# Performance work log

Measured on AMD Instinct MI355X. Metric: run time of the kernel, lower is better.

## Reference

```python
import jax, jax.numpy as jnp
import numpy as np

B, S, D = 1, 2048, 2048
NH, NKV, HD = 32, 8, 64
EPS = 1e-5
SCALE = float(HD) ** 0.5


def _rope(x, cos, sin):
    # x: [b, h, s, hd]; cos/sin: [s, hd//2]; interleaved-pair rotary (executorch style)
    xr = x[..., 0::2]
    xi = x[..., 1::2]
    c = cos[None, None, :, :]
    s = sin[None, None, :, :]
    out_r = xr * c - xi * s
    out_i = xr * s + xi * c
    return jnp.stack([out_r, out_i], axis=-1).reshape(x.shape)


def _rmsnorm(x, w):
    var = jnp.mean(x * x, axis=-1, keepdims=True)
    return x * jax.lax.rsqrt(var + EPS) * w


def setup_inputs() -> dict:
    key = jax.random.key(0)
    ks = jax.random.split(key, 6)
    hidden_states = jax.random.normal(ks[0], (B, S, D), dtype=jnp.float32)
    # standard Llama rope tables, theta=10000
    inv_freq = 1.0 / (10000.0 ** (np.arange(0, HD, 2, dtype=np.float32) / HD))
    t = np.arange(S, dtype=np.float32)
    ang = np.outer(t, inv_freq)  # [S, HD//2]
    freqs_cos = jnp.asarray(np.cos(ang), dtype=jnp.float32)
    freqs_sin = jnp.asarray(np.sin(ang), dtype=jnp.float32)
    # additive causal mask [1,1,S,S]
    causal = jnp.tril(jnp.ones((S, S), dtype=bool))
    atten_mask = jnp.where(causal, 0.0, -1e9).astype(jnp.float32)[None, None]
    sd = 1.0 / np.sqrt(D)
    wq = jax.random.normal(ks[1], (NH * HD, D), dtype=jnp.float32) * sd
    wk = jax.random.normal(ks[2], (NKV * HD, D), dtype=jnp.float32) * sd
    wv = jax.random.normal(ks[3], (NKV * HD, D), dtype=jnp.float32) * sd
    wo = jax.random.normal(ks[4], (D, NH * HD), dtype=jnp.float32) * sd
    q_norm_w = jnp.ones((HD,), dtype=jnp.float32)
    k_norm_w = jnp.ones((HD,), dtype=jnp.float32)
    return dict(hidden_states=hidden_states, freqs_cos=freqs_cos, freqs_sin=freqs_sin,
                atten_mask=atten_mask, wq=wq, wk=wk, wv=wv, wo=wo,
                q_norm_w=q_norm_w, k_norm_w=k_norm_w)


def reference(hidden_states, freqs_cos, freqs_sin, atten_mask, wq, wk, wv, wo, q_norm_w, k_norm_w):
    b, s, _ = hidden_states.shape
    n_rep = NH // NKV
    # fused QKV projections (Linear: x @ W.T)
    q = (hidden_states @ wq.T).reshape(b, s, NH, HD).transpose(0, 2, 1, 3)   # [b,nh,s,hd]
    k = (hidden_states @ wk.T).reshape(b, s, NKV, HD).transpose(0, 2, 1, 3)  # [b,nkv,s,hd]
    v = (hidden_states @ wv.T).reshape(b, s, NKV, HD).transpose(0, 2, 1, 3)
    # RoPE, then QK RMSNorm (qk_norm_before_rope=False)
    q = _rope(q, freqs_cos, freqs_sin)
    k = _rope(k, freqs_cos, freqs_sin)
    q = _rmsnorm(q, q_norm_w)
    k = _rmsnorm(k, k_norm_w)
    # no KV cache (prefill): kh = k^T, vh = v, then GQA repeat
    kh = jnp.repeat(k, n_rep, axis=1)  # [b,nh,s,hd]
    vh = jnp.repeat(v, n_rep, axis=1)
    attn = jnp.einsum('bhqd,bhkd->bhqk', q, kh) / SCALE
    attn = jax.nn.softmax(attn + atten_mask, axis=-1)
    y = jnp.einsum('bhqk,bhkd->bhqd', attn, vh)
    y = y.transpose(0, 2, 1, 3).reshape(b, s, NH * HD)
    y = y @ wo.T
    # module returns (y, [kh], [vh]); kh stored transposed (b,nh,hd,s)
    return (y, kh.transpose(0, 1, 3, 2), vh)
```

## Files before the change

kernel.cpp:

```cpp
#include <hip/hip_runtime.h>
#include <cstdint>
#include <cstddef>

#define S_   2048
#define D_   2048
#define NH_  32
#define NKV_ 8
#define HD_  64

using bf16x8 = __attribute__((ext_vector_type(8))) __bf16;
using f32x4  = __attribute__((ext_vector_type(4))) float;

#define AS_GLOBAL(p) (const __attribute__((address_space(1))) void*)(p)
#define AS_LDS(p)    (__attribute__((address_space(3))) void*)(p)

__device__ __forceinline__ float b2f(uint u) {
  union { uint u; float f; } c; c.u = u << 16; return c.f;
}

__global__ __launch_bounds__(256) void cvt_all(
    const float* __restrict__ hs, const float* __restrict__ wq,
    const float* __restrict__ wk, const float* __restrict__ wv,
    const float* __restrict__ wo,
    __bf16* __restrict__ hs_bf, __bf16* __restrict__ wq_bf,
    __bf16* __restrict__ wk_bf, __bf16* __restrict__ wv_bf,
    __bf16* __restrict__ wo_bf) {
#pragma unroll
  for (int p = 0; p < 4; ++p) {
    int i = blockIdx.x * 1024 + p * 256 + threadIdx.x;
    const float* src; __bf16* dst; int base;
    if (i < 1048576)      { src = hs; dst = hs_bf; base = 0; }
    else if (i < 2097152) { src = wq; dst = wq_bf; base = 1048576; }
    else if (i < 2359296) { src = wk; dst = wk_bf; base = 2097152; }
    else if (i < 2621440) { src = wv; dst = wv_bf; base = 2359296; }
    else                  { src = wo; dst = wo_bf; base = 2621440; }
    i -= base;
    const float4 v = reinterpret_cast<const float4*>(src)[i];
    __bf16 t[4] = {(__bf16)v.x, (__bf16)v.y, (__bf16)v.z, (__bf16)v.w};
    reinterpret_cast<uint2*>(dst)[i] = *reinterpret_cast<uint2*>(t);
  }
}

__device__ __forceinline__ void gemm_compute_step(
    const char* ldsA, const char* ldsB, f32x4 (&acc)[4][4],
    int l15, int lg, int wm, int wn) {
  bf16x8 af[4][2], bfr[4][2];
#pragma unroll
  for (int f = 0; f < 4; ++f) {
    const int arow = wm*64 + f*16 + l15;
    const int brow = wn*64 + f*16 + l15;
#pragma unroll
    for (int ks = 0; ks < 2; ++ks) {
      af[f][ks] = *reinterpret_cast<const bf16x8*>(
          ldsA + arow*128 + (((ks*4 + lg) ^ (arow & 7)) << 4));
      bfr[f][ks] = *reinterpret_cast<const bf16x8*>(
          ldsB + brow*128 + (((ks*4 + lg) ^ (brow & 7)) << 4));
    }
  }
#pragma unroll
  for (int mf = 0; mf < 4; ++mf)
#pragma unroll
    for (int nf = 0; nf < 4; ++nf) {
      acc[mf][nf] = __builtin_amdgcn_mfma_f32_16x16x32_bf16(
          af[mf][0], bfr[nf][0], acc[mf][nf], 0, 0, 0);
      acc[mf][nf] = __builtin_amdgcn_mfma_f32_16x16x32_bf16(
          af[mf][1], bfr[nf][1], acc[mf][nf], 0, 0, 0);
    }
}

template <int MODE>
__device__ __forceinline__ void gemm_tile_128_bf(
    char (*lds)[32768],
    const __bf16* __restrict__ A, const __bf16* __restrict__ B,
    __bf16* __restrict__ C, int K, int N, int m0, int n0,
    const float* __restrict__ cosT, const float* __restrict__ sinT,
    const float* __restrict__ nw) {
  const int tid = threadIdx.x;
  const int l = tid & 63;
  const int w = tid >> 6;
  const int l15 = l & 15, lg = l >> 4;
  const int wm = w >> 1, wn = w & 1;

  f32x4 acc[4][4] = {};

  const int srow   = tid >> 3;
  const int schunk = (tid & 7) ^ (srow & 7);
  const __bf16* gA = A + (size_t)(m0 + srow) * K + schunk * 8;
  const __bf16* gB = B + (size_t)(n0 + srow) * K + schunk * 8;
  const int ldst = tid * 16;
  const int nt = K >> 6;

  auto stage = [&](char* buf, int k0) {
#pragma unroll
    for (int i = 0; i < 4; ++i) {
      __builtin_amdgcn_global_load_lds(AS_GLOBAL(gA + (size_t)i*32*K + k0),
                                       AS_LDS(buf + i*4096 + ldst), 16, 0, 0);
      __builtin_amdgcn_global_load_lds(AS_GLOBAL(gB + (size_t)i*32*K + k0),
                                       AS_LDS(buf + 16384 + i*4096 + ldst), 16, 0, 0);
    }
  };

  stage(&lds[0][0], 0);
  stage(&lds[1][0], 64);

  for (int t = 0; t < nt; ++t) {
    if (t + 1 < nt) asm volatile("s_waitcnt vmcnt(8)" ::: "memory");
    else            asm volatile("s_waitcnt vmcnt(0)" ::: "memory");
    __builtin_amdgcn_s_barrier();

    gemm_compute_step(&lds[t & 1][0], &lds[t & 1][16384], acc, l15, lg, wm, wn);

    __builtin_amdgcn_s_barrier();

    if (t + 2 < nt) stage(&lds[t & 1][0], (t + 2) * 64);
  }

  if constexpr (MODE == 0) {
#pragma unroll
    for (int mf = 0; mf < 4; ++mf)
#pragma unroll
      for (int nf = 0; nf < 4; ++nf)
#pragma unroll
        for (int r = 0; r < 4; ++r)
          C[(size_t)(m0 + wm*64 + mf*16 + lg*4 + r) * N + n0 + wn*64 + nf*16 + l15]
              = (__bf16)acc[mf][nf][r];
  } else {
    const float fin = (MODE == 1) ? 0.180336880111120426f : 1.0f;
    float wv_[4];
#pragma unroll
    for (int nf = 0; nf < 4; ++nf) wv_[nf] = nw[nf*16 + l15];
    const int odd = l15 & 1;
#pragma unroll
    for (int mf = 0; mf < 4; ++mf) {
#pragma unroll
      for (int r = 0; r < 4; ++r) {
        const int row = m0 + wm*64 + mf*16 + lg*4 + r;
        float ro[4];
        float ssq = 0.f;
#pragma unroll
        for (int nf = 0; nf < 4; ++nf) {
          const float v = acc[mf][nf][r];
          const float p = __shfl_xor(v, 1);
          const int d2 = (nf*16 + l15) >> 1;
          const float c  = cosT[row*32 + d2];
          const float sn = sinT[row*32 + d2];
          ro[nf] = odd ? fmaf(p, sn, v*c) : fmaf(v, c, -p*sn);
          ssq = fmaf(ro[nf], ro[nf], ssq);
        }
        ssq += __shfl_xor(ssq, 1);
        ssq += __shfl_xor(ssq, 2);
        ssq += __shfl_xor(ssq, 4);
        ssq += __shfl_xor(ssq, 8);
        const float rinv = rsqrtf(ssq * (1.0f/64.0f) + 1e-5f);
#pragma unroll
        for (int nf = 0; nf < 4; ++nf)
          C[(size_t)row * N + n0 + wn*64 + nf*16 + l15]
              = (__bf16)(ro[nf] * rinv * wv_[nf] * fin);
      }
    }
  }
}

__device__ __forceinline__ void gemm_tile_128_d2(
    const __bf16* __restrict__ A, const __bf16* __restrict__ B,
    float* __restrict__ C, int K, int N, int m0, int n0) {
  __shared__ __align__(16) char lds[3][32768];
  const int tid = threadIdx.x;
  const int l = tid & 63;
  const int w = tid >> 6;
  const int l15 = l & 15, lg = l >> 4;
  const int wm = w >> 1, wn = w & 1;

  f32x4 acc[4][4] = {};

  const int srow   = tid >> 3;
  const int schunk = (tid & 7) ^ (srow & 7);
  const __bf16* gA = A + (size_t)(m0 + srow) * K + schunk * 8;
  const __bf16* gB = B + (size_t)(n0 + srow) * K + schunk * 8;
  const int ldst = tid * 16;
  const int nt = K >> 6;

#pragma unroll
  for (int i = 0; i < 4; ++i) {
    __builtin_amdgcn_global_load_lds(AS_GLOBAL(gA + (size_t)i*32*K),
                                     AS_LDS(&lds[0][i*4096 + ldst]), 16, 0, 0);
    __builtin_amdgcn_global_load_lds(AS_GLOBAL(gB + (size_t)i*32*K),
                                     AS_LDS(&lds[0][16384 + i*4096 + ldst]), 16, 0, 0);
  }
#pragma unroll
  for (int i = 0; i < 4; ++i) {
    __builtin_amdgcn_global_load_lds(AS_GLOBAL(gA + (size_t)i*32*K + 64),
                                     AS_LDS(&lds[1][i*4096 + ldst]), 16, 0, 0);
    __builtin_amdgcn_global_load_lds(AS_GLOBAL(gB + (size_t)i*32*K + 64),
                                     AS_LDS(&lds[1][16384 + i*4096 + ldst]), 16, 0, 0);
  }

  char* p0 = &lds[0][0];
  char* p1 = &lds[1][0];
  char* p2 = &lds[2][0];

  for (int t = 0; t < nt; ++t) {
    if (t + 1 < nt) asm volatile("s_waitcnt vmcnt(8)" ::: "memory");
    else            asm volatile("s_waitcnt vmcnt(0)" ::: "memory");
    __builtin_amdgcn_s_barrier();

    if (t + 2 < nt) {
      const int k0 = (t + 2) * 64;
#pragma unroll
      for (int i = 0; i < 4; ++i) {
        __builtin_amdgcn_global_load_lds(AS_GLOBAL(gA + (size_t)i*32*K + k0),
                                         AS_LDS(p2 + i*4096 + ldst), 16, 0, 0);
        __builtin_amdgcn_global_load_lds(AS_GLOBAL(gB + (size_t)i*32*K + k0),
                                         AS_LDS(p2 + 16384 + i*4096 + ldst), 16, 0, 0);
      }
    }

    gemm_compute_step(p0, p0 + 16384, acc, l15, lg, wm, wn);

    char* tmp = p0; p0 = p1; p1 = p2; p2 = tmp;
  }

#pragma unroll
  for (int mf = 0; mf < 4; ++mf)
#pragma unroll
    for (int nf = 0; nf < 4; ++nf)
#pragma unroll
      for (int r = 0; r < 4; ++r)
        C[(size_t)(m0 + wm*64 + mf*16 + lg*4 + r) * N + n0 + wn*64 + nf*16 + l15]
            = acc[mf][nf][r];
}

__global__ __launch_bounds__(256) void gemm_qkv(
    const __bf16* __restrict__ hs,
    const __bf16* __restrict__ wq, const __bf16* __restrict__ wk,
    const __bf16* __restrict__ wv,
    __bf16* __restrict__ qbf, __bf16* __restrict__ kbf, __bf16* __restrict__ vp,
    const float* __restrict__ fcos, const float* __restrict__ fsin,
    const float* __restrict__ qw, const float* __restrict__ kw) {
  __shared__ __align__(16) char lds[2][32768];
  const int bx = blockIdx.x;
  const int m0 = blockIdx.y * 128;
  if (bx < 16) {
    gemm_tile_128_bf<1>(lds, hs, wq, qbf, 2048, 2048, m0, bx*128, fcos, fsin, qw);
  } else if (bx < 20) {
    gemm_tile_128_bf<2>(lds, hs, wk, kbf, 2048, 512, m0, (bx-16)*128, fcos, fsin, kw);
  } else {
    gemm_tile_128_bf<0>(lds, hs, wv, vp, 2048, 512, m0, (bx-20)*128,
                        nullptr, nullptr, nullptr);
  }
}

__global__ __launch_bounds__(256) void gemm_wo(
    const __bf16* __restrict__ ypre, const __bf16* __restrict__ wo,
    float* __restrict__ y) {
  gemm_tile_128_d2(ypre, wo, y, 2048, 2048, blockIdx.y * 128, blockIdx.x * 128);
}

__global__ __launch_bounds__(256) void transpose_kv(
    const __bf16* __restrict__ kpost, float* __restrict__ khT,
    const __bf16* __restrict__ vp, float* __restrict__ vh,
    __bf16* __restrict__ vtbf) {
  __shared__ float tl[64][68];
  const int kvh = blockIdx.y;
  const int t = threadIdx.x;
  if (blockIdx.x < 32) {
    const int s0 = blockIdx.x * 64;
    {
      const int d0 = (t & 15) * 4;
      const int sl = t >> 4;
#pragma unroll
      for (int rep = 0; rep < 4; ++rep) {
        const int srow = sl + rep*16;
        const uint2 v = *reinterpret_cast<const uint2*>(
            &kpost[(size_t)(s0 + srow)*(NKV_*HD_) + kvh*HD_ + d0]);
        tl[d0+0][srow] = b2f(v.x & 0xffff);
        tl[d0+1][srow] = b2f(v.x >> 16);
        tl[d0+2][srow] = b2f(v.y & 0xffff);
        tl[d0+3][srow] = b2f(v.y >> 16);
      }
    }
    __syncthreads();
    {
      const int d  = t >> 2;
      const int s4 = (t & 3) * 16;
#pragma unroll
      for (int c = 0; c < 4; ++c) {
        float4 v;
        v.x = tl[d][s4+c*4+0]; v.y = tl[d][s4+c*4+1];
        v.z = tl[d][s4+c*4+2]; v.w = tl[d][s4+c*4+3];
#pragma unroll
        for (int r = 0; r < 4; ++r) {
          *reinterpret_cast<float4*>(
              &khT[((size_t)(kvh*4 + r)*HD_ + d)*S_ + s0 + s4 + c*4]) = v;
        }
      }
    }
  } else {
    const int s0 = (blockIdx.x - 32) * 64;
    const int srow = t >> 2, dc = (t & 3) * 16;
    const __bf16* src = &vp[(size_t)(s0 + srow)*(NKV_*HD_) + kvh*HD_ + dc];
    const uint4 a = reinterpret_cast<const uint4*>(src)[0];
    const uint4 b = reinterpret_cast<const uint4*>(src)[1];
    float f[16];
    f[0]=b2f(a.x&0xffff); f[1]=b2f(a.x>>16); f[2]=b2f(a.y&0xffff); f[3]=b2f(a.y>>16);
    f[4]=b2f(a.z&0xffff); f[5]=b2f(a.z>>16); f[6]=b2f(a.w&0xffff); f[7]=b2f(a.w>>16);
    f[8]=b2f(b.x&0xffff); f[9]=b2f(b.x>>16); f[10]=b2f(b.y&0xffff); f[11]=b2f(b.y>>16);
    f[12]=b2f(b.z&0xffff); f[13]=b2f(b.z>>16); f[14]=b2f(b.w&0xffff); f[15]=b2f(b.w>>16);
#pragma unroll
    for (int i = 0; i < 16; ++i) tl[srow][dc + i] = f[i];
#pragma unroll
    for (int r = 0; r < 4; ++r) {
      float* dst = &vh[((size_t)(kvh*4 + r)*S_ + s0 + srow)*HD_ + dc];
#pragma unroll
      for (int cc = 0; cc < 4; ++cc) {
        float4 v4 = {f[cc*4+0], f[cc*4+1], f[cc*4+2], f[cc*4+3]};
        reinterpret_cast<float4*>(dst)[cc] = v4;
      }
    }
    __syncthreads();
    const int dr = t >> 2, sc = (t & 3) * 16;
    __bf16 vals[16];
#pragma unroll
    for (int i = 0; i < 16; ++i) vals[i] = (__bf16)tl[sc + i][dr];
    uint4* dst = reinterpret_cast<uint4*>(&vtbf[((size_t)(kvh*64 + dr))*S_ + s0 + sc]);
    dst[0] = reinterpret_cast<uint4*>(vals)[0];
    dst[1] = reinterpret_cast<uint4*>(vals)[1];
  }
}

__device__ __forceinline__ uint pack2bf(float a, float b) {
  __bf16 x = (__bf16)a, y = (__bf16)b;
  const uint ux = (uint)*reinterpret_cast<ushort*>(&x);
  const uint uy = (uint)*reinterpret_cast<ushort*>(&y);
  return ux | (uy << 16);
}

__device__ __forceinline__ float max3f(float a, float b, float c) {
  return fmaxf(fmaxf(a, b), c);
}

__device__ __forceinline__ void qk_tile_T(
    const char* kldh, bf16x8 qf0, bf16x8 qf1, f32x4 (&s_)[4],
    int l15, int lg) {
  __builtin_amdgcn_s_setprio(1);
#pragma unroll
  for (int nb = 0; nb < 4; ++nb) {
    const int row = nb*16 + l15;
    const int bc  = lg*16;
    const bf16x8 kb0 = *reinterpret_cast<const bf16x8*>(
        kldh + row*128 + ((bc)      ^ ((row & 7) << 4)));
    const bf16x8 kb1 = *reinterpret_cast<const bf16x8*>(
        kldh + row*128 + ((bc + 64) ^ ((row & 7) << 4)));
    f32x4 t = f32x4{0.f, 0.f, 0.f, 0.f};
    t = __builtin_amdgcn_mfma_f32_16x16x32_bf16(kb0, qf0, t, 0, 0, 0);
    t = __builtin_amdgcn_mfma_f32_16x16x32_bf16(kb1, qf1, t, 0, 0, 0);
    s_[nb] = t;
  }
  __builtin_amdgcn_s_setprio(0);
}

__device__ __forceinline__ void softmax_pv_T(
    f32x4 (&s_)[4], float& m_, float& l_, f32x4 (&o_)[4],
    char* pldw, const char* vbase, int l15, int lg) {
  const float a0 = max3f(s_[0][0], s_[0][1], s_[0][2]);
  const float a1 = max3f(s_[0][3], s_[1][0], s_[1][1]);
  const float a2 = max3f(s_[1][2], s_[1][3], s_[2][0]);
  const float a3 = max3f(s_[2][1], s_[2][2], s_[2][3]);
  const float a4 = max3f(s_[3][0], s_[3][1], s_[3][2]);
  const float b0 = max3f(a0, a1, a2);
  const float b1 = max3f(a3, a4, s_[3][3]);
  float mx = fmaxf(b0, b1);
  mx = fmaxf(mx, __shfl_xor(mx, 16));
  mx = fmaxf(mx, __shfl_xor(mx, 32));

  if (!__all(mx <= m_ + 8.f)) {
    const float mnew = fmaxf(m_, mx);
    const float scl = exp2f(m_ - mnew);
    m_ = mnew;
    l_ *= scl;
#pragma unroll
    for (int nb = 0; nb < 4; ++nb) {
      o_[nb][0] *= scl; o_[nb][1] *= scl; o_[nb][2] *= scl; o_[nb][3] *= scl;
    }
  }

  const int swz = (l15 & 7) << 4;
  float ls = 0.f;
#pragma unroll
  for (int nb = 0; nb < 4; ++nb) {
    float p0 = exp2f(s_[nb][0] - m_);
    float p1 = exp2f(s_[nb][1] - m_);
    float p2 = exp2f(s_[nb][2] - m_);
    float p3 = exp2f(s_[nb][3] - m_);
    ls += (p0 + p1) + (p2 + p3);
    uint2 pw;
    pw.x = pack2bf(p0, p1);
    pw.y = pack2bf(p2, p3);
    *reinterpret_cast<uint2*>(pldw + ((l15*128 + nb*32 + lg*8) ^ swz)) = pw;
  }
  ls += __shfl_xor(ls, 16);
  ls += __shfl_xor(ls, 32);
  l_ += ls;

  const bf16x8 pb0 = *reinterpret_cast<const bf16x8*>(
      pldw + ((l15*128 + lg*16)      ^ swz));
  const bf16x8 pb1 = *reinterpret_cast<const bf16x8*>(
      pldw + ((l15*128 + lg*16 + 64) ^ swz));

  __builtin_amdgcn_s_setprio(1);
#pragma unroll
  for (int nb = 0; nb < 4; ++nb) {
    const int row = nb*16 + l15;
    const int bc  = lg*16;
    const bf16x8 v0 = *reinterpret_cast<const bf16x8*>(
        vbase + row*128 + ((bc)      ^ ((row & 7) << 4)));
    const bf16x8 v1 = *reinterpret_cast<const bf16x8*>(
        vbase + row*128 + ((bc + 64) ^ ((row & 7) << 4)));
    f32x4 t = o_[nb];
    t = __builtin_amdgcn_mfma_f32_16x16x32_bf16(v0, pb0, t, 0, 0, 0);
    t = __builtin_amdgcn_mfma_f32_16x16x32_bf16(v1, pb1, t, 0, 0, 0);
    o_[nb] = t;
  }
  __builtin_amdgcn_s_setprio(0);
}

__device__ __forceinline__ void mask_diag_T(f32x4 (&s_)[4], int l15, int lg, int wg) {
  const int qrow = wg*16 + l15;
#pragma unroll
  for (int nb = 0; nb < 4; ++nb)
#pragma unroll
    for (int r = 0; r < 4; ++r)
      if (nb*16 + lg*4 + r > qrow) s_[nb][r] = -1e30f;
}

__global__ __launch_bounds__(512, 4) void flash_attn_mfma(
    const __bf16* __restrict__ qbf, const __bf16* __restrict__ kbf,
    const __bf16* __restrict__ vtbf, __bf16* __restrict__ ypre) {
  __shared__ __align__(16) char smem[49152];

  const int h   = blockIdx.y;
  const int pi  = blockIdx.x;
  const int qbA = pi, qbB = 31 - pi;
  const int SS  = (qbB >> 1) + 1;
  const int kvh = h >> 2;
  const int tid = threadIdx.x;
  const int l   = tid & 63;
  const int w   = tid >> 6;
  const int g   = tid >> 8;
  const int wg  = w & 3;
  const int l15 = l & 15;
  const int lg  = l >> 4;

  char* kldg = smem + g*8192;
  char* vtlg = smem + 16384 + g*8192;
  char* pldw = smem + 32768 + w*2048;

  const int ts = tid & 255;
  const int j  = ts >> 2;
  const int c0 = (ts & 3) * 16;
  const int b0 = (j*128 + c0*2)      ^ ((j & 7) << 4);
  const int b1 = (j*128 + c0*2 + 16) ^ ((j & 7) << 4);
  const __bf16* ksrc = kbf  + (size_t)(g*64 + j)*(NKV_*HD_) + kvh*HD_ + c0;
  const __bf16* vsrc = vtbf + (size_t)(kvh*64 + j)*S_ + g*64 + c0;

  bf16x8 qfA0, qfA1, qfB0, qfB1;
  {
    const __bf16* qa = qbf + (size_t)(qbA*64 + wg*16 + l15)*D_ + h*HD_ + lg*8;
    qfA0 = *reinterpret_cast<const bf16x8*>(qa);
    qfA1 = *reinterpret_cast<const bf16x8*>(qa + 32);
    const __bf16* qb = qbf + (size_t)(qbB*64 + wg*16 + l15)*D_ + h*HD_ + lg*8;
    qfB0 = *reinterpret_cast<const bf16x8*>(qb);
    qfB1 = *reinterpret_cast<const bf16x8*>(qb + 32);
  }

  f32x4 oA[4], oB[4];
#pragma unroll
  for (int nb = 0; nb < 4; ++nb) {
    oA[nb] = f32x4{0.f, 0.f, 0.f, 0.f};
    oB[nb] = f32x4{0.f, 0.f, 0.f, 0.f};
  }
  float mA = -1e30f, lA = 0.f, mB = -1e30f, lB = 0.f;

  uint4 kr0 = reinterpret_cast<const uint4*>(ksrc)[0];
  uint4 kr1 = reinterpret_cast<const uint4*>(ksrc + 8)[0];
  uint4 vr0 = reinterpret_cast<const uint4*>(vsrc)[0];
  uint4 vr1 = reinterpret_cast<const uint4*>(vsrc + 8)[0];

  for (int st = 0; st < SS; ++st) {
    __syncthreads();
    *reinterpret_cast<uint4*>(kldg + b0) = kr0;
    *reinterpret_cast<uint4*>(kldg + b1) = kr1;
    *reinterpret_cast<uint4*>(vtlg + b0) = vr0;
    *reinterpret_cast<uint4*>(vtlg + b1) = vr1;
    __syncthreads();

    if (st + 1 < SS) {
      const __bf16* kn = ksrc + (size_t)(st + 1)*128*(NKV_*HD_);
      const __bf16* vn = vsrc + (size_t)(st + 1)*128;
      kr0 = reinterpret_cast<const uint4*>(kn)[0];
      kr1 = reinterpret_cast<const uint4*>(kn + 8)[0];
      vr0 = reinterpret_cast<const uint4*>(vn)[0];
      vr1 = reinterpret_cast<const uint4*>(vn + 8)[0];
    }

    const int kt = 2*st + g;
    if (kt <= qbB) {
      f32x4 s_[4];
      qk_tile_T(kldg, qfB0, qfB1, s_, l15, lg);
      if (kt == qbB) mask_diag_T(s_, l15, lg, wg);
      softmax_pv_T(s_, mB, lB, oB, pldw, vtlg, l15, lg);
    }
    if (kt <= qbA) {
      f32x4 s_[4];
      qk_tile_T(kldg, qfA0, qfA1, s_, l15, lg);
      if (kt == qbA) mask_diag_T(s_, l15, lg, wg);
      softmax_pv_T(s_, mA, lA, oA, pldw, vtlg, l15, lg);
    }
  }

  float* ox = reinterpret_cast<float*>(smem);
  float* ml = reinterpret_cast<float*>(smem + 20480);
  float* po = ox + (wg*64 + l)*17;
  float* pm = ml + (wg*64 + l)*9;

  __syncthreads();
  if (g == 1) {
#pragma unroll
    for (int nb = 0; nb < 4; ++nb)
#pragma unroll
      for (int r = 0; r < 4; ++r) po[nb*4 + r] = oB[nb][r];
    pm[0] = mB; pm[1] = lB;
  }
  __syncthreads();
  if (g == 0) {
    const float m1 = pm[0], l1 = pm[1];
    const float m = fmaxf(mB, m1);
    const float s0 = exp2f(mB - m), s1 = exp2f(m1 - m);
    lB = lB*s0 + l1*s1;
#pragma unroll
    for (int nb = 0; nb < 4; ++nb)
#pragma unroll
      for (int r = 0; r < 4; ++r)
        oB[nb][r] = oB[nb][r]*s0 + po[nb*4 + r]*s1;
  }
  __syncthreads();
  if (g == 1) {
#pragma unroll
    for (int nb = 0; nb < 4; ++nb)
#pragma unroll
      for (int r = 0; r < 4; ++r) po[nb*4 + r] = oA[nb][r];
    pm[0] = mA; pm[1] = lA;
  }
  __syncthreads();
  if (g == 0) {
    const float m1 = pm[0], l1 = pm[1];
    const float m = fmaxf(mA, m1);
    const float s0 = exp2f(mA - m), s1 = exp2f(m1 - m);
    lA = lA*s0 + l1*s1;
#pragma unroll
    for (int nb = 0; nb < 4; ++nb)
#pragma unroll
      for (int r = 0; r < 4; ++r)
        oA[nb][r] = oA[nb][r]*s0 + po[nb*4 + r]*s1;

    const float rlA = 1.0f / lA, rlB = 1.0f / lB;
    const size_t rowA = (size_t)(qbA*64 + wg*16 + l15)*D_ + h*HD_;
    const size_t rowB = (size_t)(qbB*64 + wg*16 + l15)*D_ + h*HD_;
#pragma unroll
    for (int nb = 0; nb < 4; ++nb) {
      uint2 pa, pb;
      pa.x = pack2bf(oA[nb][0]*rlA, oA[nb][1]*rlA);
      pa.y = pack2bf(oA[nb][2]*rlA, oA[nb][3]*rlA);
      pb.x = pack2bf(oB[nb][0]*rlB, oB[nb][1]*rlB);
      pb.y = pack2bf(oB[nb][2]*rlB, oB[nb][3]*rlB);
      *reinterpret_cast<uint2*>(&ypre[rowA + nb*16 + lg*4]) = pa;
      *reinterpret_cast<uint2*>(&ypre[rowB + nb*16 + lg*4]) = pb;
    }
  }
}

extern "C" void kernel_launch(void* const* d_in, const int* in_sizes, int n_in,
                              void* d_out, int out_size, void* d_ws, size_t ws_size,
                              hipStream_t stream) {
  (void)in_sizes; (void)n_in; (void)out_size;
  const float* hs   = (const float*)d_in[0];
  const float* fcos = (const float*)d_in[1];
  const float* fsin = (const float*)d_in[2];
  const float* wq = (const float*)d_in[4];
  const float* wk = (const float*)d_in[5];
  const float* wv = (const float*)d_in[6];
  const float* wo = (const float*)d_in[7];
  const float* qw = (const float*)d_in[8];
  const float* kw = (const float*)d_in[9];

  float* out = (float*)d_out;
  float* y   = out;
  float* khT = out + 4194304;
  float* vh  = out + 8388608;

  __bf16* qbf   = (__bf16*)y;
  __bf16* kbf   = (__bf16*)((char*)y + 8*1024*1024);
  __bf16* vtbf  = (__bf16*)((char*)y + 10*1024*1024);
  __bf16* hs_bf = (__bf16*)khT;
  __bf16* wq_bf = (__bf16*)((char*)khT + 8*1024*1024);
  __bf16* wk_bf = (__bf16*)vh;
  __bf16* wv_bf = (__bf16*)((char*)vh + 2*1024*1024);

  const size_t need = (size_t)40 * 1024 * 1024;
  if (ws_size < need) return;
  char* ws = (char*)d_ws;
  __bf16* vp_bf   = (__bf16*)(ws);
  __bf16* ypre_bf = (__bf16*)(ws + 2*1024*1024);
  __bf16* wo_bf   = (__bf16*)(ws + 10*1024*1024);

  cvt_all<<<3584, 256, 0, stream>>>(hs, wq, wk, wv, wo,
                                    hs_bf, wq_bf, wk_bf, wv_bf, wo_bf);

  gemm_qkv<<<dim3(24, 16), 256, 0, stream>>>(hs_bf, wq_bf, wk_bf, wv_bf,
                                             qbf, kbf, vp_bf,
                                             fcos, fsin, qw, kw);

  transpose_kv<<<dim3(64, 8), 256, 0, stream>>>(kbf, khT, vp_bf, vh, vtbf);

  flash_attn_mfma<<<dim3(16, 32), 512, 0, stream>>>(qbf, kbf, vtbf, ypre_bf);

  gemm_wo<<<dim3(16, 16), 256, 0, stream>>>(ypre_bf, wo_bf, y);
}
```

Measured before the change: 138.5 us.

## Shrink QKV GEMM tiles to 128x64 with simpler double-buffered pipeline

Each QKV GEMM block now computes a 128x64 output tile instead of 128x128, and the grid doubles to 48x16 blocks so more CUs are busy (384 blocks before versus 768 now on a 256-CU part). Each wave owns 32 rows across the full 64 columns, and a 64-column tile is exactly one head, so the RoPE and RMSNorm epilogue reduction stays inside the tile. The prefetch scheme changes from two stages in flight with vmcnt waits to a single stage ahead with __syncthreads each step. The trade-off is more global traffic per FLOP, since A is reloaded for twice as many column tiles, and less load latency hidden per iteration.

```diff
diff --git a/kernel.cpp b/kernel.cpp
--- a/kernel.cpp
+++ b/kernel.cpp
@@ -69,8 +69,8 @@
 }
 
 template <int MODE>
-__device__ __forceinline__ void gemm_tile_128_bf(
-    char (*lds)[32768],
+__device__ __forceinline__ void gemm_tile_64_bf(
+    char (*lds)[24576],
     const __bf16* __restrict__ A, const __bf16* __restrict__ B,
     __bf16* __restrict__ C, int K, int N, int m0, int n0,
     const float* __restrict__ cosT, const float* __restrict__ sinT,
@@ -79,9 +79,8 @@
   const int l = tid & 63;
   const int w = tid >> 6;
   const int l15 = l & 15, lg = l >> 4;
-  const int wm = w >> 1, wn = w & 1;
-
-  f32x4 acc[4][4] = {};
+
+  f32x4 acc[2][4] = {};
 
   const int srow   = tid >> 3;
   const int schunk = (tid & 7) ^ (srow & 7);
@@ -92,37 +91,64 @@
 
   auto stage = [&](char* buf, int k0) {
 #pragma unroll
-    for (int i = 0; i < 4; ++i) {
+    for (int i = 0; i < 4; ++i)
       __builtin_amdgcn_global_load_lds(AS_GLOBAL(gA + (size_t)i*32*K + k0),
                                        AS_LDS(buf + i*4096 + ldst), 16, 0, 0);
+#pragma unroll
+    for (int i = 0; i < 2; ++i)
       __builtin_amdgcn_global_load_lds(AS_GLOBAL(gB + (size_t)i*32*K + k0),
                                        AS_LDS(buf + 16384 + i*4096 + ldst), 16, 0, 0);
-    }
   };
 
   stage(&lds[0][0], 0);
-  stage(&lds[1][0], 64);
-
+  __syncthreads();
+
+  int cur = 0;
   for (int t = 0; t < nt; ++t) {
-    if (t + 1 < nt) asm volatile("s_waitcnt vmcnt(8)" ::: "memory");
-    else            asm volatile("s_waitcnt vmcnt(0)" ::: "memory");
-    __builtin_amdgcn_s_barrier();
-
-    gemm_compute_step(&lds[t & 1][0], &lds[t & 1][16384], acc, l15, lg, wm, wn);
-
-    __builtin_amdgcn_s_barrier();
-
-    if (t + 2 < nt) stage(&lds[t & 1][0], (t + 2) * 64);
+    if (t + 1 < nt) stage(&lds[cur ^ 1][0], (t + 1) * 64);
+
+    {
+      const char* ldsA = &lds[cur][0];
+      const char* ldsB = &lds[cur][16384];
+      bf16x8 af[2][2], bfr[4][2];
+#pragma unroll
+      for (int f = 0; f < 2; ++f) {
+        const int arow = w*32 + f*16 + l15;
+#pragma unroll
+        for (int ks = 0; ks < 2; ++ks)
+          af[f][ks] = *reinterpret_cast<const bf16x8*>(
+              ldsA + arow*128 + (((ks*4 + lg) ^ (arow & 7)) << 4));
+      }
+#pragma unroll
+      for (int nf = 0; nf < 4; ++nf) {
+        const int brow = nf*16 + l15;
+#pragma unroll
+        for (int ks = 0; ks < 2; ++ks)
+          bfr[nf][ks] = *reinterpret_cast<const bf16x8*>(
+              ldsB + brow*128 + (((ks*4 + lg) ^ (brow & 7)) << 4));
+      }
+#pragma unroll
+      for (int mf = 0; mf < 2; ++mf)
+#pragma unroll
+        for (int nf = 0; nf < 4; ++nf) {
+          acc[mf][nf] = __builtin_amdgcn_mfma_f32_16x16x32_bf16(
+              af[mf][0], bfr[nf][0], acc[mf][nf], 0, 0, 0);
+          acc[mf][nf] = __builtin_amdgcn_mfma_f32_16x16x32_bf16(
+              af[mf][1], bfr[nf][1], acc[mf][nf], 0, 0, 0);
+        }
+    }
+    __syncthreads();
+    cur ^= 1;
   }
 
   if constexpr (MODE == 0) {
 #pragma unroll
-    for (int mf = 0; mf < 4; ++mf)
+    for (int mf = 0; mf < 2; ++mf)
 #pragma unroll
       for (int nf = 0; nf < 4; ++nf)
 #pragma unroll
         for (int r = 0; r < 4; ++r)
-          C[(size_t)(m0 + wm*64 + mf*16 + lg*4 + r) * N + n0 + wn*64 + nf*16 + l15]
+          C[(size_t)(m0 + w*32 + mf*16 + lg*4 + r) * N + n0 + nf*16 + l15]
               = (__bf16)acc[mf][nf][r];
   } else {
     const float fin = (MODE == 1) ? 0.180336880111120426f : 1.0f;
@@ -131,10 +157,10 @@
     for (int nf = 0; nf < 4; ++nf) wv_[nf] = nw[nf*16 + l15];
     const int odd = l15 & 1;
 #pragma unroll
-    for (int mf = 0; mf < 4; ++mf) {
+    for (int mf = 0; mf < 2; ++mf) {
 #pragma unroll
       for (int r = 0; r < 4; ++r) {
-        const int row = m0 + wm*64 + mf*16 + lg*4 + r;
+        const int row = m0 + w*32 + mf*16 + lg*4 + r;
         float ro[4];
         float ssq = 0.f;
 #pragma unroll
@@ -154,7 +180,7 @@
         const float rinv = rsqrtf(ssq * (1.0f/64.0f) + 1e-5f);
 #pragma unroll
         for (int nf = 0; nf < 4; ++nf)
-          C[(size_t)row * N + n0 + wn*64 + nf*16 + l15]
+          C[(size_t)row * N + n0 + nf*16 + l15]
               = (__bf16)(ro[nf] * rinv * wv_[nf] * fin);
       }
     }
@@ -237,16 +263,16 @@
     __bf16* __restrict__ qbf, __bf16* __restrict__ kbf, __bf16* __restrict__ vp,
     const float* __restrict__ fcos, const float* __restrict__ fsin,
     const float* __restrict__ qw, const float* __restrict__ kw) {
-  __shared__ __align__(16) char lds[2][32768];
+  __shared__ __align__(16) char lds[2][24576];
   const int bx = blockIdx.x;
   const int m0 = blockIdx.y * 128;
-  if (bx < 16) {
-    gemm_tile_128_bf<1>(lds, hs, wq, qbf, 2048, 2048, m0, bx*128, fcos, fsin, qw);
-  } else if (bx < 20) {
-    gemm_tile_128_bf<2>(lds, hs, wk, kbf, 2048, 512, m0, (bx-16)*128, fcos, fsin, kw);
+  if (bx < 32) {
+    gemm_tile_64_bf<1>(lds, hs, wq, qbf, 2048, 2048, m0, bx*64, fcos, fsin, qw);
+  } else if (bx < 40) {
+    gemm_tile_64_bf<2>(lds, hs, wk, kbf, 2048, 512, m0, (bx-32)*64, fcos, fsin, kw);
   } else {
-    gemm_tile_128_bf<0>(lds, hs, wv, vp, 2048, 512, m0, (bx-20)*128,
-                        nullptr, nullptr, nullptr);
+    gemm_tile_64_bf<0>(lds, hs, wv, vp, 2048, 512, m0, (bx-40)*64,
+                       nullptr, nullptr, nullptr);
   }
 }
 
@@ -616,7 +642,7 @@
   cvt_all<<<3584, 256, 0, stream>>>(hs, wq, wk, wv, wo,
                                     hs_bf, wq_bf, wk_bf, wv_bf, wo_bf);
 
-  gemm_qkv<<<dim3(24, 16), 256, 0, stream>>>(hs_bf, wq_bf, wk_bf, wv_bf,
+  gemm_qkv<<<dim3(48, 16), 256, 0, stream>>>(hs_bf, wq_bf, wk_bf, wv_bf,
                                              qbf, kbf, vp_bf,
                                              fcos, fsin, qw, kw);
 
```

Measured after the change: 132.9 us, median of 2. 1.04x faster.
